# Kernel optimization log

Hardware: AMD Instinct MI355X
Metric: run time of the kernel (lower is better)

Reference implementation:

```python
import jax, jax.numpy as jnp
import numpy as np

N = 100000      # nodes
E = 1600000     # edges
F_IN = 27       # node features
EMB = 64        # embedding size
H = 128         # hidden/out channels
L = 4           # GNN layers
G = 512         # num_graphs


def setup_inputs() -> dict:
    key = jax.random.key(0)
    ks = jax.random.split(key, 13)
    s = 0.05
    return {
        "x": jax.random.normal(ks[0], (N, F_IN), jnp.float32),
        "edge_index": jax.random.randint(ks[1], (2, E), 0, N),
        "batch": jnp.sort(jax.random.randint(ks[2], (N,), 0, G)),
        "lin0_w": jax.random.normal(ks[3], (F_IN, EMB), jnp.float32) * s,
        "ggc_weight": jax.random.normal(ks[4], (L, H, H), jnp.float32) * s,
        "gru_w_ih": jax.random.normal(ks[5], (3 * H, H), jnp.float32) * s,
        "gru_w_hh": jax.random.normal(ks[6], (3 * H, H), jnp.float32) * s,
        "gru_b_ih": jax.random.normal(ks[7], (3 * H,), jnp.float32) * s,
        "gru_b_hh": jax.random.normal(ks[8], (3 * H,), jnp.float32) * s,
        "lin1_w": jax.random.normal(ks[9], (H, 1), jnp.float32) * s,
        "lin1_b": jax.random.normal(ks[10], (1,), jnp.float32) * s,
        "lin2_w": jax.random.normal(ks[11], (H, 1), jnp.float32) * s,
        "lin2_b": jax.random.normal(ks[12], (1,), jnp.float32) * s,
    }


def _gru_cell(m, h, w_ih, w_hh, b_ih, b_hh):
    # torch.nn.GRUCell math
    gi = m @ w_ih.T + b_ih          # [N, 3H]
    gh = h @ w_hh.T + b_hh          # [N, 3H]
    i_r, i_z, i_n = jnp.split(gi, 3, axis=1)
    h_r, h_z, h_n = jnp.split(gh, 3, axis=1)
    r = jax.nn.sigmoid(i_r + h_r)
    z = jax.nn.sigmoid(i_z + h_z)
    n = jnp.tanh(i_n + r * h_n)
    return (1.0 - z) * n + z * h


def reference(x, edge_index, batch, lin0_w, ggc_weight,
              gru_w_ih, gru_w_hh, gru_b_ih, gru_b_hh,
              lin1_w, lin1_b, lin2_w, lin2_b):
    x1 = jax.nn.sigmoid(x @ lin0_w)                       # [N, EMB]
    h = jnp.pad(x1, ((0, 0), (0, H - EMB)))               # pad to out_channels
    src, dst = edge_index[0], edge_index[1]
    for i in range(L):
        m = h @ ggc_weight[i]                             # [N, H]
        m = jax.ops.segment_sum(m[src], dst, num_segments=N)  # add-aggregate at target
        h = _gru_cell(m, h, gru_w_ih, gru_w_hh, gru_b_ih, gru_b_hh)
    xr = jax.nn.relu(h)
    mu = xr @ lin1_w + lin1_b                             # [N, 1]
    sigma = jax.nn.softplus(xr @ lin2_w + lin2_b)         # [N, 1]
    uncorrected_mu = mu
    mu_all = jax.ops.segment_sum(mu, batch, num_segments=G)        # [G, 1]
    sigma_all = jax.ops.segment_sum(sigma, batch, num_segments=G)  # [G, 1]
    # vectorized per-graph correction (original loops over graphs)
    mu_c = mu - mu_all[batch] * (sigma / sigma_all[batch])
    return (mu_c.squeeze(1), x1, sigma.squeeze(1), uncorrected_mu.squeeze(1))
```

## Files before the change

### kernel.cpp

```cpp
#include <hip/hip_runtime.h>
#include <math.h>

#define NN 100000
#define FIN 27
#define EMB 64
#define HH 128
#define LAYERS 4
#define GG 512
#define SCAN_CHUNK 2048
#define SPAN 512
#define SPANSHIFT 9
#define MAXNB 256
#define ECAP 16384
#define LPAD_US 136
#define TM 64

typedef __attribute__((ext_vector_type(8))) short short8;
typedef __attribute__((ext_vector_type(4))) float floatx4;

__device__ __forceinline__ float sigmf(float x) { return 1.0f / (1.0f + __expf(-x)); }
__device__ __forceinline__ float tanhfast(float x) { return 1.0f - 2.0f / (__expf(2.0f * x) + 1.0f); }

__device__ __forceinline__ unsigned short f2bf(float f) {
    unsigned int u = __float_as_uint(f);
    u += 0x7FFFu + ((u >> 16) & 1u);
    return (unsigned short)(u >> 16);
}

__device__ __forceinline__ float bflo(unsigned int v) { return __uint_as_float(v << 16); }
__device__ __forceinline__ float bfhi(unsigned int v) { return __uint_as_float(v & 0xFFFF0000u); }
__device__ __forceinline__ float bfs(unsigned short v) { return __uint_as_float(((unsigned)v) << 16); }

__global__ void lin0_kernel(const float* __restrict__ x, const float* __restrict__ w,
                            float* __restrict__ x1_out, unsigned short* __restrict__ hbf, int n) {
    int wave = (int)((blockIdx.x * blockDim.x + threadIdx.x) >> 6);
    int lane = threadIdx.x & 63;
    if (wave >= n) return;
    const float* xr = x + (size_t)wave * FIN;
    float acc = 0.0f;
#pragma unroll
    for (int k = 0; k < FIN; ++k) acc += xr[k] * w[k * EMB + lane];
    float v = 1.0f / (1.0f + expf(-acc));
    x1_out[(size_t)wave * EMB + lane] = v;
    hbf[(size_t)wave * HH + lane] = f2bf(v);
}

__global__ void bucket_scatter_direct(const int* __restrict__ src, const int* __restrict__ dst,
                                      int* __restrict__ bucket_cnt, unsigned* __restrict__ ebuf,
                                      int e) {
    __shared__ int lh[MAXNB];
    __shared__ int gb[MAXNB];
    int t = threadIdx.x;
    for (int i = t; i < MAXNB; i += 1024) lh[i] = 0;
    __syncthreads();
    int base = blockIdx.x * 16384;
    int lidx[16], sv[16], dv[16];
#pragma unroll
    for (int i = 0; i < 16; ++i) {
        int eid = base + i * 1024 + t;
        if (eid < e) {
            sv[i] = src[eid];
            dv[i] = dst[eid];
            lidx[i] = atomicAdd(&lh[dv[i] >> SPANSHIFT], 1);
        } else lidx[i] = -1;
    }
    __syncthreads();
    for (int i = t; i < MAXNB; i += 1024) {
        int c = lh[i];
        gb[i] = c ? atomicAdd(&bucket_cnt[i], c) : 0;
    }
    __syncthreads();
#pragma unroll
    for (int i = 0; i < 16; ++i) {
        if (lidx[i] >= 0) {
            int b = dv[i] >> SPANSHIFT;
            int pos = gb[b] + lidx[i];
            if (pos < ECAP) {
                unsigned dl = (unsigned)(dv[i] - (b << SPANSHIFT));
                ebuf[(size_t)b * ECAP + pos] = (dl << 17) | (unsigned)sv[i];
            }
        }
    }
}

__global__ void deg_from_buckets(const unsigned* __restrict__ ebuf, const int* __restrict__ bucket_cnt,
                                 int* __restrict__ deg, int n) {
    __shared__ int ld[SPAN];
    int b = blockIdx.x, t = threadIdx.x;
    ld[t] = 0; ld[t + 256] = 0;
    __syncthreads();
    int cnt = bucket_cnt[b];
    if (cnt > ECAP) cnt = ECAP;
    size_t base = (size_t)b * ECAP;
    int nodebase = b << SPANSHIFT;
    for (int j = t; j < cnt; j += 256)
        atomicAdd(&ld[ebuf[base + j] >> 17], 1);
    __syncthreads();
    int i0 = nodebase + t, i1 = nodebase + 256 + t;
    if (i0 < n) deg[i0] = ld[t];
    if (i1 < n) deg[i1] = ld[t + 256];
}

__global__ void scan_partial(const int* __restrict__ deg, int* __restrict__ blocksum, int n) {
    int b = blockIdx.x, t = threadIdx.x;
    int base = b * SCAN_CHUNK + t * 8;
    int s = 0;
#pragma unroll
    for (int i = 0; i < 8; ++i) {
        int idx = base + i;
        if (idx < n) s += deg[idx];
    }
#pragma unroll
    for (int off = 32; off > 0; off >>= 1) s += __shfl_down(s, off, 64);
    __shared__ int ws[4];
    if ((t & 63) == 0) ws[t >> 6] = s;
    __syncthreads();
    if (t == 0) blocksum[b] = ws[0] + ws[1] + ws[2] + ws[3];
}

__global__ void scan_blocksums(const int* __restrict__ blocksum, int* __restrict__ blockoff, int nb) {
    int t = threadIdx.x;
    int own = (t < nb) ? blocksum[t] : 0;
    int v = own;
    for (int off = 1; off < 64; off <<= 1) {
        int u = __shfl_up(v, off, 64);
        if (t >= off) v += u;
    }
    if (t < nb) blockoff[t] = v - own;
}

__global__ void scan_final(const int* __restrict__ deg, const int* __restrict__ blockoff,
                           int* __restrict__ rowptr, int n) {
    int b = blockIdx.x, t = threadIdx.x;
    int base = b * SCAN_CHUNK + t * 8;
    int v[8];
    int s = 0;
#pragma unroll
    for (int i = 0; i < 8; ++i) {
        int idx = base + i;
        v[i] = (idx < n) ? deg[idx] : 0;
        s += v[i];
    }
    __shared__ int ts[256];
    ts[t] = s;
    __syncthreads();
    for (int off = 1; off < 256; off <<= 1) {
        int u = (t >= off) ? ts[t - off] : 0;
        __syncthreads();
        ts[t] += u;
        __syncthreads();
    }
    int run = blockoff[b] + ((t == 0) ? 0 : ts[t - 1]);
#pragma unroll
    for (int i = 0; i < 8; ++i) {
        int idx = base + i;
        if (idx < n) {
            rowptr[idx] = run;
            run += v[i];
        } else if (idx == n) {
            rowptr[n] = run;
        }
    }
}

__global__ void place_kernel(const unsigned* __restrict__ ebuf, const int* __restrict__ bucket_cnt,
                             const int* __restrict__ rowptr, int* __restrict__ col, int n) {
    __shared__ int cur[SPAN];
    int b = blockIdx.x, t = threadIdx.x;
    int nodebase = b << SPANSHIFT;
    int i0 = nodebase + t, i1 = nodebase + 256 + t;
    cur[t] = (i0 < n) ? rowptr[i0] : 0;
    cur[t + 256] = (i1 < n) ? rowptr[i1] : 0;
    __syncthreads();
    int cnt = bucket_cnt[b];
    if (cnt > ECAP) cnt = ECAP;
    size_t base = (size_t)b * ECAP;
    for (int j = t; j < cnt; j += 256) {
        unsigned ed = ebuf[base + j];
        int pos = atomicAdd(&cur[ed >> 17], 1);
        col[pos] = (int)(ed & 0x1FFFFu);
    }
}

template <int HALF>
__global__ __launch_bounds__(512, 8)
void agg_kernel(const unsigned short* __restrict__ hin, unsigned short* __restrict__ aggout,
                const int* __restrict__ rowptr, const int* __restrict__ col, int n) {
    int node = (int)((blockIdx.x * blockDim.x + threadIdx.x) >> 6);
    int lane = threadIdx.x & 63;
    if (node >= n) return;
    int l16 = lane & 15;
    int lg = lane >> 4;
    const uint4* hin4 = (const uint4*)hin;
    const uint2* hin2 = (const uint2*)hin;
    int r0 = rowptr[node];
    int r1 = rowptr[node + 1];

    if (HALF) {
        float a[4], b[4];
#pragma unroll
        for (int k = 0; k < 4; ++k) { a[k] = 0.0f; b[k] = 0.0f; }
        int j = r0 + lg;
        for (; j + 4 < r1; j += 8) {
            int s0 = col[j], s1 = col[j + 4];
            uint2 v0 = hin2[(size_t)s0 * 32 + l16];
            uint2 v1 = hin2[(size_t)s1 * 32 + l16];
            a[0] += bflo(v0.x); a[1] += bfhi(v0.x);
            a[2] += bflo(v0.y); a[3] += bfhi(v0.y);
            b[0] += bflo(v1.x); b[1] += bfhi(v1.x);
            b[2] += bflo(v1.y); b[3] += bfhi(v1.y);
        }
        for (; j < r1; j += 4) {
            int s = col[j];
            uint2 v = hin2[(size_t)s * 32 + l16];
            a[0] += bflo(v.x); a[1] += bfhi(v.x);
            a[2] += bflo(v.y); a[3] += bfhi(v.y);
        }
#pragma unroll
        for (int k = 0; k < 4; ++k) {
            a[k] += b[k];
            a[k] += __shfl_xor(a[k], 32, 64);
            a[k] += __shfl_xor(a[k], 16, 64);
        }
        if (lg == 0) {
            uint2 o;
            o.x = (unsigned)f2bf(a[0]) | ((unsigned)f2bf(a[1]) << 16);
            o.y = (unsigned)f2bf(a[2]) | ((unsigned)f2bf(a[3]) << 16);
            *(uint2*)(aggout + (size_t)node * HH + l16 * 4) = o;
        }
    } else {
        float a[8], b[8];
#pragma unroll
        for (int k = 0; k < 8; ++k) { a[k] = 0.0f; b[k] = 0.0f; }
        int j = r0 + lg;
        for (; j + 12 < r1; j += 16) {
            int s0 = col[j], s1 = col[j + 4], s2 = col[j + 8], s3 = col[j + 12];
            uint4 v0 = hin4[(size_t)s0 * 16 + l16];
            uint4 v1 = hin4[(size_t)s1 * 16 + l16];
            uint4 v2 = hin4[(size_t)s2 * 16 + l16];
            uint4 v3 = hin4[(size_t)s3 * 16 + l16];
            a[0] += bflo(v0.x); a[1] += bfhi(v0.x);
            a[2] += bflo(v0.y); a[3] += bfhi(v0.y);
            a[4] += bflo(v0.z); a[5] += bfhi(v0.z);
            a[6] += bflo(v0.w); a[7] += bfhi(v0.w);
            b[0] += bflo(v1.x); b[1] += bfhi(v1.x);
            b[2] += bflo(v1.y); b[3] += bfhi(v1.y);
            b[4] += bflo(v1.z); b[5] += bfhi(v1.z);
            b[6] += bflo(v1.w); b[7] += bfhi(v1.w);
            a[0] += bflo(v2.x); a[1] += bfhi(v2.x);
            a[2] += bflo(v2.y); a[3] += bfhi(v2.y);
            a[4] += bflo(v2.z); a[5] += bfhi(v2.z);
            a[6] += bflo(v2.w); a[7] += bfhi(v2.w);
            b[0] += bflo(v3.x); b[1] += bfhi(v3.x);
            b[2] += bflo(v3.y); b[3] += bfhi(v3.y);
            b[4] += bflo(v3.z); b[5] += bfhi(v3.z);
            b[6] += bflo(v3.w); b[7] += bfhi(v3.w);
        }
        for (; j + 4 < r1; j += 8) {
            int s0 = col[j], s1 = col[j + 4];
            uint4 v0 = hin4[(size_t)s0 * 16 + l16];
            uint4 v1 = hin4[(size_t)s1 * 16 + l16];
            a[0] += bflo(v0.x); a[1] += bfhi(v0.x);
            a[2] += bflo(v0.y); a[3] += bfhi(v0.y);
            a[4] += bflo(v0.z); a[5] += bfhi(v0.z);
            a[6] += bflo(v0.w); a[7] += bfhi(v0.w);
            b[0] += bflo(v1.x); b[1] += bfhi(v1.x);
            b[2] += bflo(v1.y); b[3] += bfhi(v1.y);
            b[4] += bflo(v1.z); b[5] += bfhi(v1.z);
            b[6] += bflo(v1.w); b[7] += bfhi(v1.w);
        }
        for (; j < r1; j += 4) {
            int s = col[j];
            uint4 v = hin4[(size_t)s * 16 + l16];
            a[0] += bflo(v.x); a[1] += bfhi(v.x);
            a[2] += bflo(v.y); a[3] += bfhi(v.y);
            a[4] += bflo(v.z); a[5] += bfhi(v.z);
            a[6] += bflo(v.w); a[7] += bfhi(v.w);
        }
#pragma unroll
        for (int k = 0; k < 8; ++k) {
            a[k] += b[k];
            a[k] += __shfl_xor(a[k], 32, 64);
            a[k] += __shfl_xor(a[k], 16, 64);
        }
        if (lg == 0) {
            uint4 o;
            o.x = (unsigned)f2bf(a[0]) | ((unsigned)f2bf(a[1]) << 16);
            o.y = (unsigned)f2bf(a[2]) | ((unsigned)f2bf(a[3]) << 16);
            o.z = (unsigned)f2bf(a[4]) | ((unsigned)f2bf(a[5]) << 16);
            o.w = (unsigned)f2bf(a[6]) | ((unsigned)f2bf(a[7]) << 16);
            *(uint4*)(aggout + (size_t)node * HH + l16 * 8) = o;
        }
    }
}

template <int HALF>
__global__ __launch_bounds__(1024, 4)
void gru_kernel(const unsigned short* __restrict__ aggin,
                const unsigned short* __restrict__ hin,
                unsigned short* __restrict__ hout,
                const unsigned short* __restrict__ Wfp,
                const unsigned short* __restrict__ whhp,
                const float* __restrict__ b_ih, const float* __restrict__ b_hh,
                int n) {
    __shared__ unsigned short aggL[TM * LPAD_US];
    __shared__ unsigned short hL[TM * LPAD_US];
    int wave = threadIdx.x >> 6;
    int lane = threadIdx.x & 63;
    int quad = lane >> 4;
    int l15 = lane & 15;
    int w8 = wave & 7;
    int mg = wave >> 3;
    int M0 = blockIdx.x * TM;
    if (M0 >= n) return;

    {
        int row = threadIdx.x >> 4;
        int q = threadIdx.x & 15;
        int gr = M0 + row;
        uint4 va = make_uint4(0, 0, 0, 0), vh = va;
        if (gr < n && !(HALF && q >= 8)) {
            va = ((const uint4*)aggin)[(size_t)gr * 16 + q];
            vh = ((const uint4*)hin)[(size_t)gr * 16 + q];
        }
        *(uint4*)(&aggL[row * LPAD_US + q * 8]) = va;
        *(uint4*)(&hL[row * LPAD_US + q * 8]) = vh;
    }
    __syncthreads();

    floatx4 gi[2][3], gh[2][3];
#pragma unroll
    for (int m = 0; m < 2; ++m)
#pragma unroll
        for (int g = 0; g < 3; ++g) {
            gi[m][g] = (floatx4)0.0f;
            gh[m][g] = (floatx4)0.0f;
        }

    const int KTMAX = HALF ? 2 : 4;
#pragma unroll
    for (int kt = 0; kt < KTMAX; ++kt) {
        int kbase = kt * 32 + quad * 8;
        short8 aA[2], aH[2];
#pragma unroll
        for (int m = 0; m < 2; ++m) {
            int rt = (mg * 2 + m) * 16 + l15;
            aA[m] = *(const short8*)(&aggL[rt * LPAD_US + kbase]);
            aH[m] = *(const short8*)(&hL[rt * LPAD_US + kbase]);
        }
#pragma unroll
        for (int g = 0; g < 3; ++g) {
            int ct = g * 8 + w8;
            size_t boff = ((size_t)(kt * 24 + ct) * 64 + lane) * 8;
            short8 bi = *(const short8*)(Wfp + boff);
            short8 bh = *(const short8*)(whhp + boff);
#pragma unroll
            for (int m = 0; m < 2; ++m) {
                gi[m][g] = __builtin_amdgcn_mfma_f32_16x16x32_bf16(aA[m], bi, gi[m][g], 0, 0, 0);
                gh[m][g] = __builtin_amdgcn_mfma_f32_16x16x32_bf16(aH[m], bh, gh[m][g], 0, 0, 0);
            }
        }
    }

    __syncthreads();

    {
        int c = w8 * 16 + l15;
        float bir = b_ih[c], biz = b_ih[128 + c], bin_ = b_ih[256 + c];
        float bhr = b_hh[c], bhz = b_hh[128 + c], bhn = b_hh[256 + c];
#pragma unroll
        for (int m = 0; m < 2; ++m) {
#pragma unroll
            for (int j = 0; j < 4; ++j) {
                int row = (mg * 2 + m) * 16 + quad * 4 + j;
                int lidx = row * LPAD_US + c;
                float gir = gi[m][0][j] + bir;
                float ghr = gh[m][0][j] + bhr;
                float giz = gi[m][1][j] + biz;
                float ghz = gh[m][1][j] + bhz;
                float gin = gi[m][2][j] + bin_;
                float ghn = gh[m][2][j] + bhn;
                float rr = sigmf(gir + ghr);
                float zz = sigmf(giz + ghz);
                float nn = tanhfast(gin + rr * ghn);
                float hp = bfs(hL[lidx]);
                aggL[lidx] = f2bf((1.0f - zz) * nn + zz * hp);
            }
        }
    }

    __syncthreads();

    {
        int row = threadIdx.x >> 4;
        int q = threadIdx.x & 15;
        int gr = M0 + row;
        if (gr < n) {
            uint4 v = *(const uint4*)(&aggL[row * LPAD_US + q * 8]);
            *(uint4*)(hout + (size_t)gr * HH + q * 8) = v;
        }
    }
}

__global__ void pack_whh(const float* __restrict__ w_hh, unsigned short* __restrict__ whhp) {
    int id = blockIdx.x * blockDim.x + threadIdx.x;
    if (id >= 4 * 24 * 64 * 8) return;
    int j = id & 7;
    int lane = (id >> 3) & 63;
    int ctkt = id >> 9;
    int ct = ctkt % 24;
    int kt = ctkt / 24;
    int k = kt * 32 + (lane >> 4) * 8 + j;
    int col = ct * 16 + (lane & 15);
    whhp[id] = f2bf(w_hh[col * HH + k]);
}

__global__ void pack_wf(const float* __restrict__ ggc, const float* __restrict__ w_ih,
                        unsigned short* __restrict__ Wfp) {
    int id = blockIdx.x * blockDim.x + threadIdx.x;
    if (id >= LAYERS * 4 * 24 * 64 * 8) return;
    int l = id / 49152;
    int rem = id % 49152;
    int j = rem & 7;
    int lane = (rem >> 3) & 63;
    int ctkt = rem >> 9;
    int ct = ctkt % 24;
    int kt = ctkt / 24;
    int k = kt * 32 + (lane >> 4) * 8 + j;
    int col = ct * 16 + (lane & 15);
    const float4* gr = (const float4*)(ggc + ((size_t)l * HH + k) * HH);
    const float4* wr = (const float4*)(w_ih + (size_t)col * HH);
    float acc = 0.0f;
#pragma unroll 4
    for (int q = 0; q < HH / 4; ++q) {
        float4 g = gr[q], w = wr[q];
        acc += g.x * w.x + g.y * w.y + g.z * w.z + g.w * w.w;
    }
    Wfp[id] = f2bf(acc);
}

__global__ void readout_kernel(const unsigned int* __restrict__ h2, const float* __restrict__ w1,
                               const float* __restrict__ b1, const float* __restrict__ w2,
                               const float* __restrict__ b2,
                               float* __restrict__ out_mu, float* __restrict__ out_sg, int n) {
    int wave = (int)((blockIdx.x * blockDim.x + threadIdx.x) >> 6);
    int lane = threadIdx.x & 63;
    if (wave >= n) return;
    unsigned int u = h2[(size_t)wave * 64 + lane];
    float x0 = fmaxf(bflo(u), 0.0f);
    float x1 = fmaxf(bfhi(u), 0.0f);
    float2 wv1 = ((const float2*)w1)[lane];
    float2 wv2 = ((const float2*)w2)[lane];
    float a1 = x0 * wv1.x + x1 * wv1.y;
    float a2 = x0 * wv2.x + x1 * wv2.y;
#pragma unroll
    for (int off = 32; off > 0; off >>= 1) {
        a1 += __shfl_down(a1, off, 64);
        a2 += __shfl_down(a2, off, 64);
    }
    if (lane == 0) {
        float mu = a1 + b1[0];
        float x2 = a2 + b2[0];
        float sg = (x2 > 20.0f) ? x2 : __logf(1.0f + __expf(x2));
        out_mu[wave] = mu;
        out_sg[wave] = sg;
    }
}

__device__ __forceinline__ int lbound(const int* __restrict__ a, int n, int v) {
    int lo = 0, hi = n;
    while (lo < hi) {
        int m = (lo + hi) >> 1;
        if (a[m] < v) lo = m + 1; else hi = m;
    }
    return lo;
}

__global__ void seg_correct_kernel(const float* __restrict__ out_mu, const float* __restrict__ out_sg,
                                   const int* __restrict__ batch, float* __restrict__ out_muc, int n) {
    int g = blockIdx.x;
    int lo = lbound(batch, n, g);
    int hi = lbound(batch, n, g + 1);
    float smu = 0.0f, ssg = 0.0f;
    for (int i = lo + threadIdx.x; i < hi; i += blockDim.x) {
        smu += out_mu[i];
        ssg += out_sg[i];
    }
#pragma unroll
    for (int off = 32; off > 0; off >>= 1) {
        smu += __shfl_down(smu, off, 64);
        ssg += __shfl_down(ssg, off, 64);
    }
    __shared__ float pm[4], ps[4];
    int wave = threadIdx.x >> 6;
    int lane = threadIdx.x & 63;
    if (lane == 0) { pm[wave] = smu; ps[wave] = ssg; }
    __syncthreads();
    float tot_mu = pm[0] + pm[1] + pm[2] + pm[3];
    float tot_sg = ps[0] + ps[1] + ps[2] + ps[3];
    for (int i = lo + threadIdx.x; i < hi; i += blockDim.x) {
        out_muc[i] = out_mu[i] - tot_mu * (out_sg[i] / tot_sg);
    }
}

extern "C" void kernel_launch(void* const* d_in, const int* in_sizes, int n_in,
                              void* d_out, int out_size, void* d_ws, size_t ws_size,
                              hipStream_t stream) {
    const float* x      = (const float*)d_in[0];
    const int*   ei     = (const int*)d_in[1];
    const int*   batch  = (const int*)d_in[2];
    const float* lin0_w = (const float*)d_in[3];
    const float* ggc    = (const float*)d_in[4];
    const float* w_ih   = (const float*)d_in[5];
    const float* w_hh   = (const float*)d_in[6];
    const float* b_ih   = (const float*)d_in[7];
    const float* b_hh   = (const float*)d_in[8];
    const float* l1w    = (const float*)d_in[9];
    const float* l1b    = (const float*)d_in[10];
    const float* l2w    = (const float*)d_in[11];
    const float* l2b    = (const float*)d_in[12];

    int n = in_sizes[0] / FIN;
    int e = in_sizes[1] / 2;
    const int* src = ei;
    const int* dstp = ei + e;

    float* out = (float*)d_out;
    float* out_muc = out;
    float* out_x1  = out + n;
    float* out_sg  = out + n + (size_t)n * EMB;
    float* out_mu  = out_sg + n;

    unsigned short* hbf0 = (unsigned short*)d_ws;
    unsigned short* hbf1 = hbf0 + (size_t)n * HH;
    unsigned short* Wfp  = hbf1 + (size_t)n * HH;
    unsigned short* whhp = Wfp + (size_t)LAYERS * 49152;
    int*            deg      = (int*)(whhp + 49152 + 8);
    int*            rowptr   = deg + n;
    int*            blocksum = rowptr + n + 1;
    int*            blockoff = blocksum + 64;
    int*            bucket_cnt = blockoff + 64;
    int*            col      = bucket_cnt + MAXNB;
    unsigned*       ebuf     = (unsigned*)hbf1;

    int nbuck = (n + SPAN - 1) >> SPANSHIFT;
    hipMemsetAsync(bucket_cnt, 0, MAXNB * sizeof(int), stream);

    int wave_blocks = (n * 64 + 255) / 256;
    lin0_kernel<<<wave_blocks, 256, 0, stream>>>(x, lin0_w, out_x1, hbf0, n);

    int eb = (e + 16383) / 16384;
    bucket_scatter_direct<<<eb, 1024, 0, stream>>>(src, dstp, bucket_cnt, ebuf, e);
    deg_from_buckets<<<nbuck, 256, 0, stream>>>(ebuf, bucket_cnt, deg, n);

    int nb = (n + SCAN_CHUNK) / SCAN_CHUNK;
    scan_partial<<<nb, 256, 0, stream>>>(deg, blocksum, n);
    scan_blocksums<<<1, 64, 0, stream>>>(blocksum, blockoff, nb);
    scan_final<<<nb, 256, 0, stream>>>(deg, blockoff, rowptr, n);

    place_kernel<<<nbuck, 256, 0, stream>>>(ebuf, bucket_cnt, rowptr, col, n);

    pack_whh<<<(49152 + 255) / 256, 256, 0, stream>>>(w_hh, whhp);
    pack_wf<<<(LAYERS * 49152 + 255) / 256, 256, 0, stream>>>(ggc, w_ih, Wfp);

    int node_wave_blocks = (n + 7) / 8;
    int gru_blocks = (n + TM - 1) / TM;
    unsigned short* hin = hbf0;
    unsigned short* hother = hbf1;
    for (int l = 0; l < LAYERS; ++l) {
        if (l == 0) {
            agg_kernel<1><<<node_wave_blocks, 512, 0, stream>>>(hin, hother, rowptr, col, n);
            gru_kernel<1><<<gru_blocks, 1024, 0, stream>>>(hother, hin, hother,
                                                           Wfp, whhp, b_ih, b_hh, n);
        } else {
            agg_kernel<0><<<node_wave_blocks, 512, 0, stream>>>(hin, hother, rowptr, col, n);
            gru_kernel<0><<<gru_blocks, 1024, 0, stream>>>(hother, hin, hother,
                                                           Wfp + (size_t)l * 49152, whhp,
                                                           b_ih, b_hh, n);
        }
        unsigned short* t = hin; hin = hother; hother = t;
    }

    readout_kernel<<<wave_blocks, 256, 0, stream>>>((const unsigned int*)hin, l1w, l1b, l2w, l2b,
                                                    out_mu, out_sg, n);
    seg_correct_kernel<<<GG, 256, 0, stream>>>(out_mu, out_sg, batch, out_muc, n);
}
```

Baseline: 687.9 us.

## Stage GRU weight slices through double-buffered LDS, read activations directly

The GRU kernel now streams packed weight k-slices (w_ih and w_hh alternating) into a double-buffered shared-memory array, with the next slice prefetched into registers while MFMAs run on the current one. Activation A fragments are loaded straight from global memory instead of being staged in LDS first, and the previous hidden state is also re-read from global for the gate update. This cuts redundant per-wave global weight reads, at the cost of a barrier per slice and uncoalesced global A loads. In HALF mode the upper half of the K range of hin is skipped on the assumption that those columns are zero.

```diff
diff --git a/kernel.cpp b/kernel.cpp
--- a/kernel.cpp
+++ b/kernel.cpp
@@ -303,10 +303,10 @@
                 const unsigned short* __restrict__ whhp,
                 const float* __restrict__ b_ih, const float* __restrict__ b_hh,
                 int n) {
-    __shared__ unsigned short aggL[TM * LPAD_US];
-    __shared__ unsigned short hL[TM * LPAD_US];
-    int wave = threadIdx.x >> 6;
-    int lane = threadIdx.x & 63;
+    __shared__ unsigned short Bb[2][12288];
+    int tid = threadIdx.x;
+    int wave = tid >> 6;
+    int lane = tid & 63;
     int quad = lane >> 4;
     int l15 = lane & 15;
     int w8 = wave & 7;
@@ -314,19 +314,8 @@
     int M0 = blockIdx.x * TM;
     if (M0 >= n) return;
 
-    {
-        int row = threadIdx.x >> 4;
-        int q = threadIdx.x & 15;
-        int gr = M0 + row;
-        uint4 va = make_uint4(0, 0, 0, 0), vh = va;
-        if (gr < n && !(HALF && q >= 8)) {
-            va = ((const uint4*)aggin)[(size_t)gr * 16 + q];
-            vh = ((const uint4*)hin)[(size_t)gr * 16 + q];
-        }
-        *(uint4*)(&aggL[row * LPAD_US + q * 8]) = va;
-        *(uint4*)(&hL[row * LPAD_US + q * 8]) = vh;
-    }
-    __syncthreads();
+    const int KTMAX = HALF ? 2 : 4;
+    const int NSLICE = 2 * KTMAX;
 
     floatx4 gi[2][3], gh[2][3];
 #pragma unroll
@@ -337,33 +326,49 @@
             gh[m][g] = (floatx4)0.0f;
         }
 
-    const int KTMAX = HALF ? 2 : 4;
-#pragma unroll
-    for (int kt = 0; kt < KTMAX; ++kt) {
-        int kbase = kt * 32 + quad * 8;
-        short8 aA[2], aH[2];
-#pragma unroll
-        for (int m = 0; m < 2; ++m) {
-            int rt = (mg * 2 + m) * 16 + l15;
-            aA[m] = *(const short8*)(&aggL[rt * LPAD_US + kbase]);
-            aH[m] = *(const short8*)(&hL[rt * LPAD_US + kbase]);
-        }
+    int ra0 = min(M0 + mg * 32 + l15, n - 1);
+    int ra1 = min(M0 + mg * 32 + 16 + l15, n - 1);
+
+    uint4 r0, r1;
+    {
+        const uint4* s4 = (const uint4*)Wfp;
+        r0 = s4[tid];
+        if (tid < 512) r1 = s4[tid + 1024];
+    }
+
+#pragma unroll
+    for (int s = 0; s < NSLICE; ++s) {
+        unsigned short* db = Bb[s & 1];
+        *(uint4*)(db + (size_t)tid * 8) = r0;
+        if (tid < 512) *(uint4*)(db + (size_t)(tid + 1024) * 8) = r1;
+        __syncthreads();
+        if (s + 1 < NSLICE) {
+            const unsigned short* nsrc = (((s + 1) & 1) ? whhp : Wfp) + ((s + 1) >> 1) * 12288;
+            const uint4* s4 = (const uint4*)nsrc;
+            r0 = s4[tid];
+            if (tid < 512) r1 = s4[tid + 1024];
+        }
+        int mat = s & 1, kt = s >> 1;
+        const unsigned short* ab = mat ? hin : aggin;
+        size_t ko = (size_t)kt * 32 + quad * 8;
+        short8 a0 = *(const short8*)(ab + (size_t)ra0 * HH + ko);
+        short8 a1 = *(const short8*)(ab + (size_t)ra1 * HH + ko);
 #pragma unroll
         for (int g = 0; g < 3; ++g) {
             int ct = g * 8 + w8;
-            size_t boff = ((size_t)(kt * 24 + ct) * 64 + lane) * 8;
-            short8 bi = *(const short8*)(Wfp + boff);
-            short8 bh = *(const short8*)(whhp + boff);
-#pragma unroll
-            for (int m = 0; m < 2; ++m) {
-                gi[m][g] = __builtin_amdgcn_mfma_f32_16x16x32_bf16(aA[m], bi, gi[m][g], 0, 0, 0);
-                gh[m][g] = __builtin_amdgcn_mfma_f32_16x16x32_bf16(aH[m], bh, gh[m][g], 0, 0, 0);
+            short8 bf = *(const short8*)(db + ct * 512 + lane * 8);
+            if (mat == 0) {
+                gi[0][g] = __builtin_amdgcn_mfma_f32_16x16x32_bf16(a0, bf, gi[0][g], 0, 0, 0);
+                gi[1][g] = __builtin_amdgcn_mfma_f32_16x16x32_bf16(a1, bf, gi[1][g], 0, 0, 0);
+            } else {
+                gh[0][g] = __builtin_amdgcn_mfma_f32_16x16x32_bf16(a0, bf, gh[0][g], 0, 0, 0);
+                gh[1][g] = __builtin_amdgcn_mfma_f32_16x16x32_bf16(a1, bf, gh[1][g], 0, 0, 0);
             }
         }
-    }
-
-    __syncthreads();
-
+        __syncthreads();
+    }
+
+    unsigned short* stg = Bb[0];
     {
         int c = w8 * 16 + l15;
         float bir = b_ih[c], biz = b_ih[128 + c], bin_ = b_ih[256 + c];
@@ -372,8 +377,10 @@
         for (int m = 0; m < 2; ++m) {
 #pragma unroll
             for (int j = 0; j < 4; ++j) {
-                int row = (mg * 2 + m) * 16 + quad * 4 + j;
-                int lidx = row * LPAD_US + c;
+                int row = mg * 32 + m * 16 + quad * 4 + j;
+                int gr = min(M0 + row, n - 1);
+                float hp = 0.0f;
+                if (!HALF || w8 < 4) hp = bfs(hin[(size_t)gr * HH + c]);
                 float gir = gi[m][0][j] + bir;
                 float ghr = gh[m][0][j] + bhr;
                 float giz = gi[m][1][j] + biz;
@@ -383,20 +390,18 @@
                 float rr = sigmf(gir + ghr);
                 float zz = sigmf(giz + ghz);
                 float nn = tanhfast(gin + rr * ghn);
-                float hp = bfs(hL[lidx]);
-                aggL[lidx] = f2bf((1.0f - zz) * nn + zz * hp);
+                stg[row * LPAD_US + c] = f2bf((1.0f - zz) * nn + zz * hp);
             }
         }
     }
-
     __syncthreads();
 
     {
-        int row = threadIdx.x >> 4;
-        int q = threadIdx.x & 15;
+        int row = tid >> 4;
+        int q = tid & 15;
         int gr = M0 + row;
         if (gr < n) {
-            uint4 v = *(const uint4*)(&aggL[row * LPAD_US + q * 8]);
+            uint4 v = *(const uint4*)(stg + row * LPAD_US + q * 8);
             *(uint4*)(hout + (size_t)gr * HH + q * 8) = v;
         }
     }
```

Result: slower. 855.5 us (+24.4%).
